# Kernel optimization log

Measured on AMD Instinct MI355X. Metric: run time of the kernel, lower is better.

Reference implementation:

```python
import jax, jax.numpy as jnp
import numpy as np

N_NODES = 50000
X_DIM = 64
EMBED_DIM = 320  # x_dim + hidden*num_hops = 64 + 128*2
N_EDGES = 400000
HIDDEN_MLP = 64
SAMPLE_BIAS = 0.0


def setup_inputs() -> dict:
    key = jax.random.key(0)
    ks = jax.random.split(key, 8)
    x = jax.random.normal(ks[0], (N_NODES, X_DIM), dtype=jnp.float32)
    embed = jax.random.normal(ks[1], (N_NODES, EMBED_DIM), dtype=jnp.float32)
    edge_index = jax.random.randint(ks[2], (2, N_EDGES), 0, N_NODES, dtype=jnp.int64)
    eps = jax.random.uniform(ks[3], (N_EDGES,), dtype=jnp.float32)
    in_channels = 3 * EMBED_DIM
    W1 = jax.random.normal(ks[4], (in_channels, HIDDEN_MLP), dtype=jnp.float32) / np.sqrt(in_channels)
    b1 = jnp.zeros((HIDDEN_MLP,), dtype=jnp.float32)
    W2 = jax.random.normal(ks[5], (HIDDEN_MLP, 1), dtype=jnp.float32) / np.sqrt(HIDDEN_MLP)
    b2 = jnp.zeros((1,), dtype=jnp.float32)
    return {
        'x': x, 'embed': embed, 'edge_index': edge_index, 'node_id': 12345,
        'tmp': jnp.ones((), dtype=jnp.float32), 'eps': eps,
        'W1': W1, 'b1': b1, 'W2': W2, 'b2': b2,
    }


def reference(x, embed, edge_index, node_id, tmp, eps, W1, b1, W2, b2):
    # col, row = edge_index (note: source unpacks col first)
    col = edge_index[0]
    row = edge_index[1]
    E = col.shape[0]
    # gather + concat: [E, 3*embed_dim]
    center = jnp.broadcast_to(embed[node_id][None, :], (E, embed.shape[1]))
    h = jnp.concatenate([embed[col], embed[row], center], axis=-1)
    # 2-layer MLP -> per-edge logit w
    h = jax.nn.relu(h @ W1 + b1)
    w = (h @ W2 + b2).reshape(-1)
    # concrete (Gumbel-sigmoid) relaxation, training=True path
    bias = SAMPLE_BIAS + 0.0001
    e = eps * (1.0 - 2.0 * bias) + bias
    gate = (jnp.log(e) - jnp.log1p(-e) + w) / tmp
    return jax.nn.sigmoid(gate)
```

## Files before the change

kernel.cpp:

```cpp
#include <hip/hip_runtime.h>
#include <math.h>
#include <stdint.h>

#define N_NODES   50000
#define EMBED_DIM 320
#define N_EDGES   400000
#define HID       64

typedef __bf16 bf16x8 __attribute__((ext_vector_type(8)));
typedef float  f32x4  __attribute__((ext_vector_type(4)));

__device__ __forceinline__ void async_copy16(void* lds_dst, const void* g_src) {
    __builtin_amdgcn_global_load_lds(
        (const __attribute__((address_space(1))) uint32_t*)g_src,
        (__attribute__((address_space(3))) uint32_t*)lds_dst,
        16, 0, 0);
}

__global__ __launch_bounds__(256) void prep_b(const float* __restrict__ W1,
                                              const float* __restrict__ b1,
                                              const int* __restrict__ node_id,
                                              const float* __restrict__ E,
                                              __bf16* __restrict__ Bg,
                                              float* __restrict__ cterm_g) {
    if (blockIdx.x < 20) {
        int chunk = blockIdx.x * 256 + threadIdx.x;
        int l  = chunk & 63;
        int sf = chunk >> 6;
        int f  = sf & 7, s = sf >> 3;
        int c  = f * 16 + (l & 15);
        int k0 = s * 32 + (l >> 4) * 8;
        const float* src = W1 + ((size_t)k0 + (c >= 64 ? EMBED_DIM : 0)) * HID + (c & 63);
        __bf16* dst = Bg + (size_t)chunk * 8;
        #pragma unroll
        for (int j = 0; j < 8; ++j) dst[j] = (__bf16)src[(size_t)j * HID];
    } else {
        __shared__ float red[4][64];
        const int tid = threadIdx.x;
        const int j = tid & 63;
        const int g = tid >> 6;
        const int nid = node_id[0];
        const float* erow = E + (size_t)nid * EMBED_DIM;
        float s = 0.f;
        #pragma unroll 4
        for (int k = g * 80; k < (g + 1) * 80; ++k)
            s = fmaf(erow[k], W1[(size_t)(2 * EMBED_DIM + k) * HID + j], s);
        red[g][j] = s;
        __syncthreads();
        if (tid < 64)
            cterm_g[tid] = b1[tid] + red[0][tid] + red[1][tid] + red[2][tid] + red[3][tid];
    }
}

__global__ __launch_bounds__(256) void node_gemm(const float* __restrict__ E,
                                                 const __bf16* __restrict__ Bg,
                                                 const float* __restrict__ cterm_g,
                                                 __bf16* __restrict__ P) {
    __shared__ float sA[64 * EMBED_DIM];

    const int tid  = threadIdx.x;
    const int wave = tid >> 6;
    const int lane = tid & 63;
    const int r16  = lane & 15;
    const int kg   = lane >> 4;
    const int m0   = blockIdx.x * 64;

    #pragma unroll
    for (int it = 0; it < 20; ++it) {
        int g   = it * 256 + tid;
        int r   = g / 80;
        int cw  = g - r * 80;
        int scw = cw ^ (r & 7);
        int gr  = m0 + r;
        if (gr > N_NODES - 1) gr = N_NODES - 1;
        async_copy16((char*)sA + (size_t)g * 16,
                     E + (size_t)gr * EMBED_DIM + scw * 4);
    }

    float ct[4];
    #pragma unroll
    for (int f = 0; f < 4; ++f) ct[f] = cterm_g[f * 16 + r16];

    const __bf16* bbase = Bg + (size_t)lane * 8;
    bf16x8 bB[4][8];
    #pragma unroll
    for (int s = 0; s < 4; ++s)
        #pragma unroll
        for (int f = 0; f < 8; ++f)
            bB[s][f] = *(const bf16x8*)(bbase + (size_t)(s * 8 + f) * 512);

    f32x4 acc[8] = {};

    asm volatile("s_waitcnt vmcnt(0)" ::: "memory");
    __syncthreads();

    const int rt      = wave * 16 + r16;
    const int rowbase = rt * EMBED_DIM;
    #pragma unroll
    for (int s = 0; s < 10; ++s) {
        int cb = s * 8 + kg * 2;
        int c0 = cb ^ (r16 & 7);
        int c1 = (cb + 1) ^ (r16 & 7);
        f32x4 lo = *(const f32x4*)&sA[rowbase + c0 * 4];
        f32x4 hi = *(const f32x4*)&sA[rowbase + c1 * 4];
        bf16x8 av;
        av[0] = (__bf16)lo[0]; av[1] = (__bf16)lo[1];
        av[2] = (__bf16)lo[2]; av[3] = (__bf16)lo[3];
        av[4] = (__bf16)hi[0]; av[5] = (__bf16)hi[1];
        av[6] = (__bf16)hi[2]; av[7] = (__bf16)hi[3];
        #pragma unroll
        for (int f = 0; f < 8; ++f)
            acc[f] = __builtin_amdgcn_mfma_f32_16x16x32_bf16(av, bB[s & 3][f], acc[f], 0, 0, 0);
        if (s < 6) {
            #pragma unroll
            for (int f = 0; f < 8; ++f)
                bB[s & 3][f] = *(const bf16x8*)(bbase + (size_t)((s + 4) * 8 + f) * 512);
        }
    }

    const int m0w = m0 + wave * 16;
    #pragma unroll
    for (int f = 0; f < 8; ++f) {
        float c = (f < 4) ? ct[f] : 0.f;
        #pragma unroll
        for (int j = 0; j < 4; ++j) {
            int gr = m0w + kg * 4 + j;
            if (gr < N_NODES)
                P[(size_t)gr * 128 + f * 16 + r16] = (__bf16)(acc[f][j] + c);
        }
    }
}

__global__ __launch_bounds__(256) void edge_kernel(const int* __restrict__ eidx,
                                                   const float* __restrict__ eps,
                                                   const __bf16* __restrict__ P,
                                                   const float* __restrict__ W2,
                                                   const float* __restrict__ b2,
                                                   const float* __restrict__ tmp,
                                                   float* __restrict__ out) {
    const int gid = blockIdx.x * blockDim.x + threadIdx.x;
    const int e   = gid >> 3;
    const int q   = gid & 7;
    if (e >= N_EDGES) return;

    int col = eidx[e];
    int row = eidx[N_EDGES + e];
    col = min(max(col, 0), N_NODES - 1);
    row = min(max(row, 0), N_NODES - 1);

    bf16x8 a = *(const bf16x8*)(P + (size_t)col * 128 + q * 8);
    bf16x8 c = *(const bf16x8*)(P + (size_t)row * 128 + 64 + q * 8);
    float4 w0 = *(const float4*)(W2 + q * 8);
    float4 w1 = *(const float4*)(W2 + q * 8 + 4);

    float s = 0.f;
    s = fmaf(fmaxf((float)a[0] + (float)c[0], 0.f), w0.x, s);
    s = fmaf(fmaxf((float)a[1] + (float)c[1], 0.f), w0.y, s);
    s = fmaf(fmaxf((float)a[2] + (float)c[2], 0.f), w0.z, s);
    s = fmaf(fmaxf((float)a[3] + (float)c[3], 0.f), w0.w, s);
    s = fmaf(fmaxf((float)a[4] + (float)c[4], 0.f), w1.x, s);
    s = fmaf(fmaxf((float)a[5] + (float)c[5], 0.f), w1.y, s);
    s = fmaf(fmaxf((float)a[6] + (float)c[6], 0.f), w1.z, s);
    s = fmaf(fmaxf((float)a[7] + (float)c[7], 0.f), w1.w, s);

    s += __shfl_xor(s, 1);
    s += __shfl_xor(s, 2);
    s += __shfl_xor(s, 4);

    if (q == 0) {
        float w  = s + b2[0];
        const float bias = 0.0001f;
        float ee = eps[e] * (1.0f - 2.0f * bias) + bias;
        float gate = (logf(ee) - log1pf(-ee) + w) / tmp[0];
        out[e] = 1.0f / (1.0f + expf(-gate));
    }
}

extern "C" void kernel_launch(void* const* d_in, const int* in_sizes, int n_in,
                              void* d_out, int out_size, void* d_ws, size_t ws_size,
                              hipStream_t stream) {
    const float* embed = (const float*)d_in[1];
    const int*   eidx  = (const int*)d_in[2];
    const int*   nid   = (const int*)d_in[3];
    const float* tmp   = (const float*)d_in[4];
    const float* eps   = (const float*)d_in[5];
    const float* W1    = (const float*)d_in[6];
    const float* b1    = (const float*)d_in[7];
    const float* W2    = (const float*)d_in[8];
    const float* b2    = (const float*)d_in[9];
    float*       out   = (float*)d_out;

    __bf16* P       = (__bf16*)d_ws;
    __bf16* Bg      = (__bf16*)((char*)d_ws + (size_t)N_NODES * 128 * sizeof(__bf16));
    float*  cterm_g = (float*)((char*)Bg + (size_t)5120 * 8 * sizeof(__bf16));

    prep_b<<<21, 256, 0, stream>>>(W1, b1, nid, embed, Bg, cterm_g);

    int gemm_blocks = (N_NODES + 63) / 64;
    node_gemm<<<gemm_blocks, 256, 0, stream>>>(embed, Bg, cterm_g, P);

    int edge_threads = N_EDGES * 8;
    edge_kernel<<<(edge_threads + 255) / 256, 256, 0, stream>>>(
        eidx, eps, P, W2, b2, tmp, out);
}
```

Before: 148.3 us.

## Split node GEMM tile to 32 rows with waves sharing column halves

The node GEMM block tile shrinks from 64 rows to 32 rows, cutting shared memory from 80KB to 40KB and doubling the number of blocks. The four waves are now arranged as 2 row groups by 2 column groups, so each wave keeps only 4 B fragments and 4 accumulators instead of 8. Launch bounds request 4 blocks per CU. The aim is higher occupancy and lower register pressure so the async embed loads are better hidden. The cost is that each B fragment is loaded for half as many rows.

```diff
diff --git a/kernel.cpp b/kernel.cpp
--- a/kernel.cpp
+++ b/kernel.cpp
@@ -52,21 +52,23 @@
     }
 }
 
-__global__ __launch_bounds__(256) void node_gemm(const float* __restrict__ E,
-                                                 const __bf16* __restrict__ Bg,
-                                                 const float* __restrict__ cterm_g,
-                                                 __bf16* __restrict__ P) {
-    __shared__ float sA[64 * EMBED_DIM];
+__global__ __launch_bounds__(256, 4) void node_gemm(const float* __restrict__ E,
+                                                    const __bf16* __restrict__ Bg,
+                                                    const float* __restrict__ cterm_g,
+                                                    __bf16* __restrict__ P) {
+    __shared__ float sA[32 * EMBED_DIM];
 
     const int tid  = threadIdx.x;
     const int wave = tid >> 6;
     const int lane = tid & 63;
     const int r16  = lane & 15;
     const int kg   = lane >> 4;
-    const int m0   = blockIdx.x * 64;
-
-    #pragma unroll
-    for (int it = 0; it < 20; ++it) {
+    const int rowg = wave & 1;
+    const int colg = wave >> 1;
+    const int m0   = blockIdx.x * 32;
+
+    #pragma unroll
+    for (int it = 0; it < 10; ++it) {
         int g   = it * 256 + tid;
         int r   = g / 80;
         int cw  = g - r * 80;
@@ -79,23 +81,23 @@
 
     float ct[4];
     #pragma unroll
-    for (int f = 0; f < 4; ++f) ct[f] = cterm_g[f * 16 + r16];
-
-    const __bf16* bbase = Bg + (size_t)lane * 8;
-    bf16x8 bB[4][8];
+    for (int fi = 0; fi < 4; ++fi)
+        ct[fi] = (colg == 0) ? cterm_g[fi * 16 + r16] : 0.f;
+
+    const __bf16* bbase = Bg + (size_t)colg * 2048 + (size_t)lane * 8;
+    bf16x8 bB[4][4];
     #pragma unroll
     for (int s = 0; s < 4; ++s)
         #pragma unroll
-        for (int f = 0; f < 8; ++f)
-            bB[s][f] = *(const bf16x8*)(bbase + (size_t)(s * 8 + f) * 512);
-
-    f32x4 acc[8] = {};
+        for (int fi = 0; fi < 4; ++fi)
+            bB[s][fi] = *(const bf16x8*)(bbase + (size_t)(s * 8 + fi) * 512);
+
+    f32x4 acc[4] = {};
 
     asm volatile("s_waitcnt vmcnt(0)" ::: "memory");
     __syncthreads();
 
-    const int rt      = wave * 16 + r16;
-    const int rowbase = rt * EMBED_DIM;
+    const int rowbase = (rowg * 16 + r16) * EMBED_DIM;
     #pragma unroll
     for (int s = 0; s < 10; ++s) {
         int cb = s * 8 + kg * 2;
@@ -109,24 +111,23 @@
         av[4] = (__bf16)hi[0]; av[5] = (__bf16)hi[1];
         av[6] = (__bf16)hi[2]; av[7] = (__bf16)hi[3];
         #pragma unroll
-        for (int f = 0; f < 8; ++f)
-            acc[f] = __builtin_amdgcn_mfma_f32_16x16x32_bf16(av, bB[s & 3][f], acc[f], 0, 0, 0);
+        for (int fi = 0; fi < 4; ++fi)
+            acc[fi] = __builtin_amdgcn_mfma_f32_16x16x32_bf16(av, bB[s & 3][fi], acc[fi], 0, 0, 0);
         if (s < 6) {
             #pragma unroll
-            for (int f = 0; f < 8; ++f)
-                bB[s & 3][f] = *(const bf16x8*)(bbase + (size_t)((s + 4) * 8 + f) * 512);
+            for (int fi = 0; fi < 4; ++fi)
+                bB[s & 3][fi] = *(const bf16x8*)(bbase + (size_t)((s + 4) * 8 + fi) * 512);
         }
     }
 
-    const int m0w = m0 + wave * 16;
-    #pragma unroll
-    for (int f = 0; f < 8; ++f) {
-        float c = (f < 4) ? ct[f] : 0.f;
+    const int m0w = m0 + rowg * 16;
+    #pragma unroll
+    for (int fi = 0; fi < 4; ++fi) {
         #pragma unroll
         for (int j = 0; j < 4; ++j) {
             int gr = m0w + kg * 4 + j;
             if (gr < N_NODES)
-                P[(size_t)gr * 128 + f * 16 + r16] = (__bf16)(acc[f][j] + c);
+                P[(size_t)gr * 128 + colg * 64 + fi * 16 + r16] = (__bf16)(acc[fi][j] + ct[fi]);
         }
     }
 }
@@ -196,7 +197,7 @@
 
     prep_b<<<21, 256, 0, stream>>>(W1, b1, nid, embed, Bg, cterm_g);
 
-    int gemm_blocks = (N_NODES + 63) / 64;
+    int gemm_blocks = (N_NODES + 31) / 32;
     node_gemm<<<gemm_blocks, 256, 0, stream>>>(embed, Bg, cterm_g, P);
 
     int edge_threads = N_EDGES * 8;
```

After: 145.8 us. Within noise of the previous version (-1.7%).

## Stage weight tiles in LDS and load activations directly into registers

Applied to the files above, without the earlier changes.

The node GEMM now copies the bf16 weight matrix (80 KB) into LDS asynchronously. Each lane reads its embedding row slices straight from global memory into registers, so the 80 KB float activation tile no longer goes through LDS. Weight fragments are read from LDS inside the MFMA loop instead of being streamed from global memory, and launch bounds request 2 blocks per SM. The aim is to overlap the A loads with the B staging and to cut redundant global weight reads. In exchange, each block must copy the full weight matrix, and the per-lane A loads with an 8-byte stride across k-groups may be less coalesced.

```diff
diff --git a/kernel.cpp b/kernel.cpp
--- a/kernel.cpp
+++ b/kernel.cpp
@@ -52,11 +52,11 @@
     }
 }
 
-__global__ __launch_bounds__(256) void node_gemm(const float* __restrict__ E,
-                                                 const __bf16* __restrict__ Bg,
-                                                 const float* __restrict__ cterm_g,
-                                                 __bf16* __restrict__ P) {
-    __shared__ float sA[64 * EMBED_DIM];
+__global__ __launch_bounds__(256, 2) void node_gemm(const float* __restrict__ E,
+                                                    const __bf16* __restrict__ Bg,
+                                                    const float* __restrict__ cterm_g,
+                                                    __bf16* __restrict__ P) {
+    __shared__ __bf16 sB[5120 * 8];
 
     const int tid  = threadIdx.x;
     const int wave = tid >> 6;
@@ -64,61 +64,51 @@
     const int r16  = lane & 15;
     const int kg   = lane >> 4;
     const int m0   = blockIdx.x * 64;
+    const int m0w  = m0 + wave * 16;
 
     #pragma unroll
     for (int it = 0; it < 20; ++it) {
-        int g   = it * 256 + tid;
-        int r   = g / 80;
-        int cw  = g - r * 80;
-        int scw = cw ^ (r & 7);
-        int gr  = m0 + r;
-        if (gr > N_NODES - 1) gr = N_NODES - 1;
-        async_copy16((char*)sA + (size_t)g * 16,
-                     E + (size_t)gr * EMBED_DIM + scw * 4);
+        int g = it * 256 + tid;
+        async_copy16((char*)sB + (size_t)g * 16, (const char*)Bg + (size_t)g * 16);
     }
+    __builtin_amdgcn_sched_barrier(0);
 
     float ct[4];
     #pragma unroll
-    for (int f = 0; f < 4; ++f) ct[f] = cterm_g[f * 16 + r16];
+    for (int fi = 0; fi < 4; ++fi) ct[fi] = cterm_g[fi * 16 + r16];
 
-    const __bf16* bbase = Bg + (size_t)lane * 8;
-    bf16x8 bB[4][8];
-    #pragma unroll
-    for (int s = 0; s < 4; ++s)
-        #pragma unroll
-        for (int f = 0; f < 8; ++f)
-            bB[s][f] = *(const bf16x8*)(bbase + (size_t)(s * 8 + f) * 512);
+    int arow_i = m0w + r16;
+    if (arow_i > N_NODES - 1) arow_i = N_NODES - 1;
+    const float* arow = E + (size_t)arow_i * EMBED_DIM + kg * 8;
 
-    f32x4 acc[8] = {};
-
-    asm volatile("s_waitcnt vmcnt(0)" ::: "memory");
-    __syncthreads();
-
-    const int rt      = wave * 16 + r16;
-    const int rowbase = rt * EMBED_DIM;
+    float4 aA[10][2];
     #pragma unroll
     for (int s = 0; s < 10; ++s) {
-        int cb = s * 8 + kg * 2;
-        int c0 = cb ^ (r16 & 7);
-        int c1 = (cb + 1) ^ (r16 & 7);
-        f32x4 lo = *(const f32x4*)&sA[rowbase + c0 * 4];
-        f32x4 hi = *(const f32x4*)&sA[rowbase + c1 * 4];
+        aA[s][0] = *(const float4*)(arow + s * 32 + 0);
+        aA[s][1] = *(const float4*)(arow + s * 32 + 4);
+    }
+    __builtin_amdgcn_sched_barrier(0);
+
+    asm volatile("s_waitcnt vmcnt(20)" ::: "memory");
+    __builtin_amdgcn_sched_barrier(0);
+    __builtin_amdgcn_s_barrier();
+
+    const __bf16* bb = sB + (size_t)lane * 8;
+    f32x4 acc[8] = {};
+    #pragma unroll
+    for (int s = 0; s < 10; ++s) {
         bf16x8 av;
-        av[0] = (__bf16)lo[0]; av[1] = (__bf16)lo[1];
-        av[2] = (__bf16)lo[2]; av[3] = (__bf16)lo[3];
-        av[4] = (__bf16)hi[0]; av[5] = (__bf16)hi[1];
-        av[6] = (__bf16)hi[2]; av[7] = (__bf16)hi[3];
+        av[0] = (__bf16)aA[s][0].x; av[1] = (__bf16)aA[s][0].y;
+        av[2] = (__bf16)aA[s][0].z; av[3] = (__bf16)aA[s][0].w;
+        av[4] = (__bf16)aA[s][1].x; av[5] = (__bf16)aA[s][1].y;
+        av[6] = (__bf16)aA[s][1].z; av[7] = (__bf16)aA[s][1].w;
         #pragma unroll
-        for (int f = 0; f < 8; ++f)
-            acc[f] = __builtin_amdgcn_mfma_f32_16x16x32_bf16(av, bB[s & 3][f], acc[f], 0, 0, 0);
-        if (s < 6) {
-            #pragma unroll
-            for (int f = 0; f < 8; ++f)
-                bB[s & 3][f] = *(const bf16x8*)(bbase + (size_t)((s + 4) * 8 + f) * 512);
+        for (int f = 0; f < 8; ++f) {
+            bf16x8 bv = *(const bf16x8*)(bb + (size_t)(s * 8 + f) * 512);
+            acc[f] = __builtin_amdgcn_mfma_f32_16x16x32_bf16(av, bv, acc[f], 0, 0, 0);
         }
     }
 
-    const int m0w = m0 + wave * 16;
     #pragma unroll
     for (int f = 0; f < 8; ++f) {
         float c = (f < 4) ? ct[f] : 0.f;
```

After: 148.8 us. No clear change (+0.3%).
